# Kernel optimization log

Measured on AMD Instinct MI355X. Metric: run time of the kernel, lower is better.

Reference implementation:

```python
import jax, jax.numpy as jnp
import numpy as np

N_E = 1024
E_DIM = 512
BETA = 0.25


def setup_inputs() -> dict:
    key = jax.random.key(0)
    k1, k2 = jax.random.split(key)
    z = jax.random.normal(k1, (16, E_DIM, 64, 64), dtype=jnp.float32)
    # nn.Embedding default init: N(0,1)
    codebook = jax.random.normal(k2, (N_E, E_DIM), dtype=jnp.float32)
    return {"z": z, "codebook": codebook}


def reference(z, codebook):
    # z: [B, C, H, W] -> [B, H, W, C]
    zp = jnp.transpose(z, (0, 2, 3, 1))
    B, H, W, C = zp.shape
    zf = zp.reshape(-1, C)  # [N, e_dim]
    d = (jnp.sum(zf * zf, axis=1, keepdims=True)
         + jnp.sum(codebook * codebook, axis=1)
         - 2.0 * zf @ codebook.T)
    idx = jnp.argmin(d, axis=1)  # [N]
    # one-hot @ codebook == gather
    z_q = codebook[idx].reshape(B, H, W, C)
    sg = jax.lax.stop_gradient
    e_latent_loss = jnp.mean((sg(z_q) - zp) ** 2)
    q_latent_loss = jnp.mean((z_q - sg(zp)) ** 2)
    codebook_loss = q_latent_loss + BETA * e_latent_loss
    # straight-through estimator
    z_q_st = zp + sg(z_q - zp)
    z_q_out = jnp.transpose(z_q_st, (0, 3, 1, 2))  # [B, C, H, W]
    indices = idx.reshape(B, 1, H, W)
    return (z_q_out, codebook_loss, indices)
```

## Files before the change

### kernel.cpp

```cpp
#include <hip/hip_runtime.h>
#include <stdint.h>

#define N_E    1024
#define E_DIM  512
#define BATCH  16
#define HW     4096
#define NROW   (BATCH * HW)
#define ZQ_SIZE (BATCH * E_DIM * HW)
#define LOSS_OFF ZQ_SIZE
#define IDX_OFF (ZQ_SIZE + 1)

typedef _Float16 half_t;
typedef __attribute__((ext_vector_type(2)))  __fp16   fp16x2;
typedef __attribute__((ext_vector_type(8)))  _Float16 frag8;
typedef __attribute__((ext_vector_type(16))) float    accv;

union U32H2 { fp16x2 h; uint32_t u; };

static __device__ inline uint32_t pack2(float a, float b) {
    U32H2 t; t.h = __builtin_amdgcn_cvt_pkrtz(a, b); return t.u;
}

static __device__ __forceinline__ void dma16(const void* g, void* l) {
    __builtin_amdgcn_global_load_lds(
        (const __attribute__((address_space(1))) void*)g,
        (__attribute__((address_space(3))) void*)l,
        16, 0, 0);
}

__global__ void k_pack(const float* __restrict__ cb,
                       uint32_t* __restrict__ cbP,
                       float* __restrict__ cn,
                       float* __restrict__ ct) {
    __shared__ float tsh[32][33];
    int bidx = blockIdx.x;
    int tid  = threadIdx.x;

    if (bidx < 128) {
        int jt = bidx & 7, ks = bidx >> 3;
        int kq = tid & 7, jb = tid >> 3;
        uint32_t* tile = cbP + (size_t)bidx * 4096;
        int sH = kq >> 1, o = (kq & 1) * 2;
        #pragma unroll
        for (int r = 0; r < 4; r++) {
            int j = jb + 32 * r;
            float4 v = *(const float4*)(cb + (size_t)(jt * 128 + j) * E_DIM + ks * 32 + kq * 4);
            uint32_t H01 = pack2(v.x, v.y);
            uint32_t H23 = pack2(v.z, v.w);
            U32H2 h01; h01.u = H01; U32H2 h23; h23.u = H23;
            uint32_t L01 = pack2(v.x - (float)h01.h.x, v.y - (float)h01.h.y);
            uint32_t L23 = pack2(v.z - (float)h23.h.x, v.w - (float)h23.h.y);
            int dH = ((sH)     ^ (j & 7)) * 4 + o;
            int dL = ((sH + 4) ^ (j & 7)) * 4 + o;
            *(uint2*)(tile + j * 32 + dH) = make_uint2(H01, H23);
            *(uint2*)(tile + j * 32 + dL) = make_uint2(L01, L23);
        }
    } else {
        int pb = bidx - 128;
        int tx = tid & 31, ty = tid >> 5;
        int jtp = pb & 31, ctl = pb >> 5;
        int j0 = jtp * 32, c0 = ctl * 32;
        #pragma unroll
        for (int i = 0; i < 4; i++) {
            int row = ty + i * 8;
            tsh[row][tx] = cb[(size_t)(j0 + row) * E_DIM + c0 + tx];
        }
        __syncthreads();
        #pragma unroll
        for (int i = 0; i < 4; i++) {
            int row = ty + i * 8;
            ct[(size_t)(c0 + row) * N_E + j0 + tx] = tsh[tx][row];
        }
        if (pb < 256) {
            int lane = tid & 63;
            int wvid = tid >> 6;
            int j = pb * 4 + wvid;
            const float* rowp = cb + (size_t)j * E_DIM;
            float s = 0.f;
            #pragma unroll
            for (int k = 0; k < E_DIM; k += 64) {
                float v = rowp[k + lane];
                s += v * v;
            }
            #pragma unroll
            for (int m = 32; m >= 1; m >>= 1) s += __shfl_xor(s, m);
            if (lane == 0) cn[j] = s;
        }
    }
}

__global__ __launch_bounds__(512, 2) void k_argmin_mfma(
        const float* __restrict__ z,
        const uint32_t* __restrict__ cbP,
        const float* __restrict__ cn,
        uint32_t* __restrict__ bestIdx) {
    __shared__ uint32_t lds[40960];

    int tid  = threadIdx.x;
    int lane = tid & 63;
    int l31  = lane & 31;
    int lh   = lane >> 5;
    int wid  = tid >> 6;
    int wm   = wid & 1;
    int wg   = wid >> 1;

    int n0 = blockIdx.x * 64;
    int b  = n0 >> 12, hw0 = n0 & 4095;

    {
        int r  = tid & 63;
        int kg = tid >> 6;
        const float* zB = z + (size_t)b * E_DIM * HW + hw0 + r;
        #pragma unroll
        for (int g = 0; g < 16; g++) {
            int ch0 = kg * 64 + g * 4;
            float v0 = zB[(size_t)(ch0    ) * HW];
            float v1 = zB[(size_t)(ch0 + 1) * HW];
            float v2 = zB[(size_t)(ch0 + 2) * HW];
            float v3 = zB[(size_t)(ch0 + 3) * HW];
            uint32_t H01 = pack2(v0, v1);
            uint32_t H23 = pack2(v2, v3);
            U32H2 h01; h01.u = H01; U32H2 h23; h23.u = H23;
            uint32_t L01 = pack2(v0 - (float)h01.h.x, v1 - (float)h01.h.y);
            uint32_t L23 = pack2(v2 - (float)h23.h.x, v3 - (float)h23.h.y);
            int chunk = ch0 >> 5;
            int kq = (ch0 & 31) >> 2;
            uint32_t* base = lds + chunk * 2048 + r * 32;
            int o = (kq & 1) * 2, sH = kq >> 1, sw = r & 7;
            *(uint2*)&base[(((sH    ) ^ sw) << 2) + o] = make_uint2(H01, H23);
            *(uint2*)&base[(((sH + 4) ^ sw) << 2) + o] = make_uint2(L01, L23);
        }
    }
    __syncthreads();

    accv acc[8];
    #pragma unroll
    for (int j = 0; j < 8; j++)
        #pragma unroll
        for (int i = 0; i < 16; i++) acc[j][i] = 0.f;

    int uoffB = wid * 2048;
    #define BSTAGE(q) do {                                                     \
        char* lb_ = (char*)(lds + 32768) + ((q) & 1) * 16384 + uoffB;          \
        const char* gb_ = (const char*)cbP + (size_t)(q) * 16384               \
                          + uoffB + lane * 16;                                 \
        dma16(gb_,        lb_);                                                \
        dma16(gb_ + 1024, lb_ + 1024);                                         \
    } while (0)

    BSTAGE(0);
    BSTAGE(1);

    int arow = wm * 32 + l31, asw = arow & 7;
    int nn   = wg * 32 + l31, nsw = nn & 7;

    #pragma unroll 1
    for (int ks = 0; ks < 16; ks++) {
        frag8 ah0, al0, ah1, al1;
        #pragma unroll
        for (int jt = 0; jt < 8; jt++) {
            int p = ks * 8 + jt;
            if (jt == 7 && ks == 15)
                asm volatile("s_waitcnt vmcnt(0)" ::: "memory");
            else
                asm volatile("s_waitcnt vmcnt(2)" ::: "memory");
            __builtin_amdgcn_s_barrier();

            if (jt == 0) {
                const uint32_t* Ac = lds + ks * 2048 + arow * 32;
                int s0 = lh, s1 = 2 + lh;
                ah0 = *(const frag8*)&Ac[((s0 ^ asw) << 2)];
                al0 = *(const frag8*)&Ac[(((s0 + 4) ^ asw) << 2)];
                ah1 = *(const frag8*)&Ac[((s1 ^ asw) << 2)];
                al1 = *(const frag8*)&Ac[(((s1 + 4) ^ asw) << 2)];
            }
            const uint32_t* Bb = lds + 32768 + (p & 1) * 4096 + nn * 32;
            frag8 bh0 = *(const frag8*)&Bb[(((    lh) ^ nsw) << 2)];
            frag8 bl0 = *(const frag8*)&Bb[(((4 + lh) ^ nsw) << 2)];
            frag8 bh1 = *(const frag8*)&Bb[(((2 + lh) ^ nsw) << 2)];
            frag8 bl1 = *(const frag8*)&Bb[(((6 + lh) ^ nsw) << 2)];

            __builtin_amdgcn_s_setprio(1);
            acc[jt] = __builtin_amdgcn_mfma_f32_32x32x16_f16(ah0, bh0, acc[jt], 0, 0, 0);
            acc[jt] = __builtin_amdgcn_mfma_f32_32x32x16_f16(ah0, bl0, acc[jt], 0, 0, 0);
            acc[jt] = __builtin_amdgcn_mfma_f32_32x32x16_f16(al0, bh0, acc[jt], 0, 0, 0);
            acc[jt] = __builtin_amdgcn_mfma_f32_32x32x16_f16(ah1, bh1, acc[jt], 0, 0, 0);
            acc[jt] = __builtin_amdgcn_mfma_f32_32x32x16_f16(ah1, bl1, acc[jt], 0, 0, 0);
            acc[jt] = __builtin_amdgcn_mfma_f32_32x32x16_f16(al1, bh1, acc[jt], 0, 0, 0);
            __builtin_amdgcn_s_setprio(0);

            asm volatile("s_waitcnt lgkmcnt(0)" ::: "memory");
            __builtin_amdgcn_s_barrier();
            if (jt < 6 || ks < 15) BSTAGE(p + 2);
        }
    }
    #undef BSTAGE

    float cnl[8];
    #pragma unroll
    for (int j = 0; j < 8; j++) cnl[j] = cn[j * 128 + wg * 32 + l31];

    unsigned long long* red = (unsigned long long*)(lds + 32768);
    #pragma unroll
    for (int r = 0; r < 16; r++) {
        float v = 1e30f; int ix = 0;
        #pragma unroll
        for (int j = 0; j < 8; j++) {
            float d = cnl[j] - 2.f * acc[j][r];
            int code = j * 128 + wg * 32 + l31;
            if (d < v) { v = d; ix = code; }
        }
        #pragma unroll
        for (int m = 1; m <= 16; m <<= 1) {
            float ov = __shfl_xor(v, m);
            int   oi = __shfl_xor(ix, m);
            if (ov < v || (ov == v && oi < ix)) { v = ov; ix = oi; }
        }
        if (l31 == r) {
            int row = wm * 32 + (r & 3) + 8 * (r >> 2) + 4 * lh;
            uint32_t s = __float_as_uint(v);
            uint32_t k32 = (s & 0x80000000u) ? ~s : (s | 0x80000000u);
            red[wg * 64 + row] = ((unsigned long long)k32 << 32) | (uint32_t)ix;
        }
    }
    __syncthreads();
    if (tid < 64) {
        unsigned long long k0 = red[tid];
        unsigned long long k1 = red[64 + tid];
        unsigned long long k2 = red[128 + tid];
        unsigned long long k3 = red[192 + tid];
        unsigned long long k = k0 < k1 ? k0 : k1;
        if (k2 < k) k = k2;
        if (k3 < k) k = k3;
        bestIdx[n0 + tid] = (uint32_t)k;
    }
}

__global__ void k_gather_loss(const float* __restrict__ z,
                              const float* __restrict__ ct,
                              const uint32_t* __restrict__ bestIdx,
                              float* __restrict__ out,
                              float* __restrict__ pl) {
    int g = blockIdx.x * blockDim.x + threadIdx.x;
    int w4 = g & 1023;
    int bc = g >> 10;
    int c  = bc & 511;
    int b  = bc >> 9;
    int n4 = b * 1024 + w4;

    uint4 iv = *(const uint4*)(bestIdx + (size_t)n4 * 4);

    const float* ctc = ct + (size_t)c * N_E;
    float4 zq;
    zq.x = ctc[iv.x]; zq.y = ctc[iv.y]; zq.z = ctc[iv.z]; zq.w = ctc[iv.w];
    float4 zv = *(const float4*)(z + (size_t)g * 4);

    float4 d;
    d.x = zq.x - zv.x; d.y = zq.y - zv.y; d.z = zq.z - zv.z; d.w = zq.w - zv.w;
    float4 o;
    o.x = zv.x + d.x; o.y = zv.y + d.y; o.z = zv.z + d.z; o.w = zv.w + d.w;
    *(float4*)(out + (size_t)g * 4) = o;

    float ls = d.x * d.x + d.y * d.y + d.z * d.z + d.w * d.w;
    #pragma unroll
    for (int m = 32; m >= 1; m >>= 1) ls += __shfl_xor(ls, m);

    __shared__ float wsum[4];
    int lane = threadIdx.x & 63, wvid = threadIdx.x >> 6;
    if (lane == 0) wsum[wvid] = ls;
    __syncthreads();
    if (threadIdx.x == 0)
        pl[blockIdx.x] = wsum[0] + wsum[1] + wsum[2] + wsum[3];

    if (c == 0) {
        float* ip = out + IDX_OFF + (size_t)n4 * 4;
        ip[0] = (float)iv.x; ip[1] = (float)iv.y;
        ip[2] = (float)iv.z; ip[3] = (float)iv.w;
    }
}

__global__ void k_final(const float* __restrict__ pl, float* __restrict__ out) {
    float s = 0.f;
    for (int i = threadIdx.x; i < 8192; i += 256) s += pl[i];
    #pragma unroll
    for (int m = 32; m >= 1; m >>= 1) s += __shfl_xor(s, m);
    __shared__ float wsum[4];
    int lane = threadIdx.x & 63, wvid = threadIdx.x >> 6;
    if (lane == 0) wsum[wvid] = s;
    __syncthreads();
    if (threadIdx.x == 0) {
        float tot = wsum[0] + wsum[1] + wsum[2] + wsum[3];
        out[LOSS_OFF] = 1.25f * tot / (float)ZQ_SIZE;
    }
}

extern "C" void kernel_launch(void* const* d_in, const int* in_sizes, int n_in,
                              void* d_out, int out_size, void* d_ws, size_t ws_size,
                              hipStream_t stream) {
    (void)in_sizes; (void)n_in; (void)out_size; (void)ws_size;
    const float* z  = (const float*)d_in[0];
    const float* cb = (const float*)d_in[1];
    float* out = (float*)d_out;

    float* cn = (float*)d_ws + 16;
    float* ct = cn + 1024;
    uint32_t* bestIdx = (uint32_t*)(ct + 512 * 1024);
    float* pl = (float*)(bestIdx + NROW);

    uint32_t* cbP = (uint32_t*)d_out;

    k_pack<<<640, 256, 0, stream>>>(cb, cbP, cn, ct);
    k_argmin_mfma<<<1024, 512, 0, stream>>>(z, cbP, cn, bestIdx);
    k_gather_loss<<<ZQ_SIZE / 4 / 256, 256, 0, stream>>>(z, ct, bestIdx, out, pl);
    k_final<<<1, 256, 0, stream>>>(pl, out);
}
```

Baseline: 493.0 us.

## Software-pipeline codebook fragment LDS reads one step ahead of MFMAs

Restructures the GEMM main loop so the B (codebook) fragments for the next step are read from LDS into registers while the current step's MFMAs run. A third DMA stage is kept in flight to match. The K loop is written as explicit per-step macro invocations, with a peeled last iteration that handles the tail wait counts. The aim is to hide LDS read latency behind matrix math, at the cost of extra VGPRs for the next-step fragments, which may raise register pressure.

```diff
diff --git a/kernel.cpp b/kernel.cpp
--- a/kernel.cpp
+++ b/kernel.cpp
@@ -148,52 +148,85 @@
         dma16(gb_ + 1024, lb_ + 1024);                                         \
     } while (0)
 
+    int arow = wm * 32 + l31, asw = arow & 7;
+    int nn   = wg * 32 + l31, nsw = nn & 7;
+
+    frag8 aH0, aL0, aH1, aL1;
+    frag8 bH0, bL0, bH1, bL1;
+    frag8 nH0, nL0, nH1, nL1;
+
     BSTAGE(0);
     BSTAGE(1);
-
-    int arow = wm * 32 + l31, asw = arow & 7;
-    int nn   = wg * 32 + l31, nsw = nn & 7;
+    asm volatile("s_waitcnt vmcnt(2)" ::: "memory");
+    __builtin_amdgcn_s_barrier();
+    {
+        const uint32_t* Bb = lds + 32768 + nn * 32;
+        bH0 = *(const frag8*)&Bb[(((    lh) ^ nsw) << 2)];
+        bL0 = *(const frag8*)&Bb[(((4 + lh) ^ nsw) << 2)];
+        bH1 = *(const frag8*)&Bb[(((2 + lh) ^ nsw) << 2)];
+        bL1 = *(const frag8*)&Bb[(((6 + lh) ^ nsw) << 2)];
+    }
+    asm volatile("s_waitcnt lgkmcnt(0)" ::: "memory");
+    __builtin_amdgcn_s_barrier();
+    BSTAGE(2);
+
+    #define PH(jt_, vm_, stage_, load_, ksA_, pb_) do {                        \
+        if (load_) {                                                           \
+            asm volatile("s_waitcnt vmcnt(" vm_ ")" ::: "memory");             \
+            __builtin_amdgcn_s_barrier();                                      \
+            if ((jt_) == 0) {                                                  \
+                const uint32_t* Ac_ = lds + (ksA_) * 2048 + arow * 32;         \
+                aH0 = *(const frag8*)&Ac_[(((    lh) ^ asw) << 2)];            \
+                aL0 = *(const frag8*)&Ac_[(((4 + lh) ^ asw) << 2)];            \
+                aH1 = *(const frag8*)&Ac_[(((2 + lh) ^ asw) << 2)];            \
+                aL1 = *(const frag8*)&Ac_[(((6 + lh) ^ asw) << 2)];            \
+            }                                                                  \
+            const uint32_t* Bb_ = lds + 32768                                  \
+                                  + (((jt_) + 1) & 1) * 4096 + nn * 32;        \
+            nH0 = *(const frag8*)&Bb_[(((    lh) ^ nsw) << 2)];                \
+            nL0 = *(const frag8*)&Bb_[(((4 + lh) ^ nsw) << 2)];                \
+            nH1 = *(const frag8*)&Bb_[(((2 + lh) ^ nsw) << 2)];                \
+            nL1 = *(const frag8*)&Bb_[(((6 + lh) ^ nsw) << 2)];                \
+        }                                                                      \
+        __builtin_amdgcn_s_setprio(1);                                         \
+        acc[jt_] = __builtin_amdgcn_mfma_f32_32x32x16_f16(aH0, bH0, acc[jt_], 0, 0, 0); \
+        acc[jt_] = __builtin_amdgcn_mfma_f32_32x32x16_f16(aH0, bL0, acc[jt_], 0, 0, 0); \
+        acc[jt_] = __builtin_amdgcn_mfma_f32_32x32x16_f16(aL0, bH0, acc[jt_], 0, 0, 0); \
+        acc[jt_] = __builtin_amdgcn_mfma_f32_32x32x16_f16(aH1, bH1, acc[jt_], 0, 0, 0); \
+        acc[jt_] = __builtin_amdgcn_mfma_f32_32x32x16_f16(aH1, bL1, acc[jt_], 0, 0, 0); \
+        acc[jt_] = __builtin_amdgcn_mfma_f32_32x32x16_f16(aL1, bH1, acc[jt_], 0, 0, 0); \
+        __builtin_amdgcn_s_setprio(0);                                         \
+        if (load_) {                                                           \
+            asm volatile("s_waitcnt lgkmcnt(0)" ::: "memory");                 \
+            __builtin_amdgcn_s_barrier();                                      \
+            if (stage_) BSTAGE((pb_) + (jt_) + 3);                             \
+            bH0 = nH0; bL0 = nL0; bH1 = nH1; bL1 = nL1;                        \
+        }                                                                      \
+    } while (0)
 
     #pragma unroll 1
-    for (int ks = 0; ks < 16; ks++) {
-        frag8 ah0, al0, ah1, al1;
-        #pragma unroll
-        for (int jt = 0; jt < 8; jt++) {
-            int p = ks * 8 + jt;
-            if (jt == 7 && ks == 15)
-                asm volatile("s_waitcnt vmcnt(0)" ::: "memory");
-            else
-                asm volatile("s_waitcnt vmcnt(2)" ::: "memory");
-            __builtin_amdgcn_s_barrier();
-
-            if (jt == 0) {
-                const uint32_t* Ac = lds + ks * 2048 + arow * 32;
-                int s0 = lh, s1 = 2 + lh;
-                ah0 = *(const frag8*)&Ac[((s0 ^ asw) << 2)];
-                al0 = *(const frag8*)&Ac[(((s0 + 4) ^ asw) << 2)];
-                ah1 = *(const frag8*)&Ac[((s1 ^ asw) << 2)];
-                al1 = *(const frag8*)&Ac[(((s1 + 4) ^ asw) << 2)];
-            }
-            const uint32_t* Bb = lds + 32768 + (p & 1) * 4096 + nn * 32;
-            frag8 bh0 = *(const frag8*)&Bb[(((    lh) ^ nsw) << 2)];
-            frag8 bl0 = *(const frag8*)&Bb[(((4 + lh) ^ nsw) << 2)];
-            frag8 bh1 = *(const frag8*)&Bb[(((2 + lh) ^ nsw) << 2)];
-            frag8 bl1 = *(const frag8*)&Bb[(((6 + lh) ^ nsw) << 2)];
-
-            __builtin_amdgcn_s_setprio(1);
-            acc[jt] = __builtin_amdgcn_mfma_f32_32x32x16_f16(ah0, bh0, acc[jt], 0, 0, 0);
-            acc[jt] = __builtin_amdgcn_mfma_f32_32x32x16_f16(ah0, bl0, acc[jt], 0, 0, 0);
-            acc[jt] = __builtin_amdgcn_mfma_f32_32x32x16_f16(al0, bh0, acc[jt], 0, 0, 0);
-            acc[jt] = __builtin_amdgcn_mfma_f32_32x32x16_f16(ah1, bh1, acc[jt], 0, 0, 0);
-            acc[jt] = __builtin_amdgcn_mfma_f32_32x32x16_f16(ah1, bl1, acc[jt], 0, 0, 0);
-            acc[jt] = __builtin_amdgcn_mfma_f32_32x32x16_f16(al1, bh1, acc[jt], 0, 0, 0);
-            __builtin_amdgcn_s_setprio(0);
-
-            asm volatile("s_waitcnt lgkmcnt(0)" ::: "memory");
-            __builtin_amdgcn_s_barrier();
-            if (jt < 6 || ks < 15) BSTAGE(p + 2);
-        }
-    }
+    for (int ks = 0; ks < 15; ks++) {
+        int pb = ks * 8;
+        PH(0, "2", true, true, ks, pb);
+        PH(1, "2", true, true, 0,  pb);
+        PH(2, "2", true, true, 0,  pb);
+        PH(3, "2", true, true, 0,  pb);
+        PH(4, "2", true, true, 0,  pb);
+        PH(5, "2", true, true, 0,  pb);
+        PH(6, "2", true, true, 0,  pb);
+        PH(7, "2", true, true, 0,  pb);
+    }
+    {
+        PH(0, "2", true,  true,  15, 120);
+        PH(1, "2", true,  true,  0,  120);
+        PH(2, "2", true,  true,  0,  120);
+        PH(3, "2", true,  true,  0,  120);
+        PH(4, "2", true,  true,  0,  120);
+        PH(5, "2", false, true,  0,  120);
+        PH(6, "0", false, true,  0,  120);
+        PH(7, "0", false, false, 0,  120);
+    }
+    #undef PH
     #undef BSTAGE
 
     float cnl[8];
```

After: 499.4 us. Within noise of the previous version (+1.3%).
